# Kernel optimization log

Measured on AMD Instinct MI355X. Metric: run time of the kernel, lower is better.

The kernel has to match this reference:

```python
import jax, jax.numpy as jnp
import numpy as np

D_MODEL = 256
EXPERT_DIM = 512
NUM_EXPERTS = 8
TOP_K = 2
SEQ_LEN = 2048
BATCH = 2


def setup_inputs() -> dict:
    key = jax.random.key(0)
    ks = jax.random.split(key, 8)
    s = 0.02
    x = jax.random.normal(ks[0], (SEQ_LEN, BATCH, D_MODEL), dtype=jnp.float32)
    # gate: torch Linear(d_model, num_experts); store as [d, E] so logits = x @ Wg + bg
    Wg = jax.random.normal(ks[1], (D_MODEL, NUM_EXPERTS), dtype=jnp.float32) * s
    bg = jax.random.normal(ks[2], (NUM_EXPERTS,), dtype=jnp.float32) * s
    bias = jnp.zeros((NUM_EXPERTS,), dtype=jnp.float32)  # dynamic routing bias
    # experts: Linear(d, h) -> ReLU -> Linear(h, d), stacked over E
    W1 = jax.random.normal(ks[3], (NUM_EXPERTS, D_MODEL, EXPERT_DIM), dtype=jnp.float32) * s
    b1 = jax.random.normal(ks[4], (NUM_EXPERTS, EXPERT_DIM), dtype=jnp.float32) * s
    W2 = jax.random.normal(ks[5], (NUM_EXPERTS, EXPERT_DIM, D_MODEL), dtype=jnp.float32) * s
    b2 = jax.random.normal(ks[6], (NUM_EXPERTS, D_MODEL), dtype=jnp.float32) * s
    return {"x": x, "Wg": Wg, "bg": bg, "bias": bias, "W1": W1, "b1": b1, "W2": W2, "b2": b2}


def reference(x, Wg, bg, bias, W1, b1, W2, b2):
    # x: [seq, batch, d] -> flatten tokens
    x_flat = x.reshape(-1, D_MODEL)                      # [T, d]
    gate_logits = x_flat @ Wg + bg + bias                # [T, E]
    topk_vals, topk_idx = jax.lax.top_k(gate_logits, TOP_K)   # [T, K]
    # torch code subtracts the row max (topk_vals[:, :1], sorted desc) then softmaxes;
    # jax.nn.softmax is the same stable computation.
    topk_w = jax.nn.softmax(topk_vals, axis=-1)          # [T, K]
    # combine weights over experts: zero for unchosen experts -> exact same math
    # as the masked gather + scatter-add in the original loop.
    combine = (jax.nn.one_hot(topk_idx, NUM_EXPERTS, dtype=x.dtype)
               * topk_w[..., None]).sum(axis=1)          # [T, E]
    h = jax.nn.relu(jnp.einsum('td,edh->teh', x_flat, W1) + b1)   # [T, E, H]
    y = jnp.einsum('teh,ehd->ted', h, W2) + b2                     # [T, E, d]
    out = jnp.einsum('ted,te->td', y, combine)                     # [T, d]
    # dropout is identity in eval mode (p applied only in training)
    return out.reshape(x.shape)
```

## Files before the change

kernel.cpp:

```cpp
#include <hip/hip_runtime.h>
#include <hip/hip_bf16.h>
#include <math.h>

#define D_MODEL 256
#define EXPERT_DIM 512
#define NUM_EXPERTS 8
#define T_TOKENS 4096
#define TM 64
#define NGB 256
#define XS_LD 264

typedef unsigned short ushort_t;
typedef short short8_t __attribute__((ext_vector_type(8)));
typedef float f32x4 __attribute__((ext_vector_type(4)));

__device__ __forceinline__ ushort_t f2bf(float f) {
    unsigned int u = __float_as_uint(f);
    u += 0x7FFFu + ((u >> 16) & 1u);
    return (ushort_t)(u >> 16);
}
__device__ __forceinline__ float bf2f(ushort_t u) {
    return __uint_as_float((unsigned int)u << 16);
}

__global__ __launch_bounds__(256) void prep_kernel(
    const float* __restrict__ x, const float* __restrict__ Wg,
    const float* __restrict__ bg, const float* __restrict__ bias,
    const float* __restrict__ W1, const float* __restrict__ W2,
    ushort_t* __restrict__ W1f, ushort_t* __restrict__ W2f,
    ushort_t* __restrict__ xb,
    int* __restrict__ gcounts, int* __restrict__ lists,
    float* __restrict__ wts, int* __restrict__ slots)
{
    __shared__ int lcount[NUM_EXPERTS];
    const int tid = threadIdx.x;

    if (blockIdx.x < NGB) {
        const int gb = blockIdx.x;
        const int r = tid >> 4;
        const int c = tid & 15;
        const int t = gb * 16 + r;
        if (tid < NUM_EXPERTS) lcount[tid] = 0;

        float xr[16];
        const float4* xp = (const float4*)(x + (size_t)t * D_MODEL + c * 16);
#pragma unroll
        for (int q = 0; q < 4; ++q) {
            float4 v = xp[q];
            xr[q * 4 + 0] = v.x; xr[q * 4 + 1] = v.y;
            xr[q * 4 + 2] = v.z; xr[q * 4 + 3] = v.w;
        }
        ushort_t o16[16];
#pragma unroll
        for (int j = 0; j < 16; ++j) o16[j] = f2bf(xr[j]);
        ushort_t* xbp = xb + (size_t)t * D_MODEL + c * 16;
        *(int4*)(xbp)     = *(int4*)(o16);
        *(int4*)(xbp + 8) = *(int4*)(o16 + 8);

        float acc[NUM_EXPERTS];
#pragma unroll
        for (int e = 0; e < NUM_EXPERTS; ++e) acc[e] = 0.f;
#pragma unroll
        for (int j = 0; j < 16; ++j) {
            const float4* wg = (const float4*)(Wg + (c * 16 + j) * NUM_EXPERTS);
            float4 w0 = wg[0], w1 = wg[1];
            float xv = xr[j];
            acc[0] += xv * w0.x; acc[1] += xv * w0.y;
            acc[2] += xv * w0.z; acc[3] += xv * w0.w;
            acc[4] += xv * w1.x; acc[5] += xv * w1.y;
            acc[6] += xv * w1.z; acc[7] += xv * w1.w;
        }
#pragma unroll
        for (int e = 0; e < NUM_EXPERTS; ++e) {
#pragma unroll
            for (int s = 1; s < 16; s <<= 1) acc[e] += __shfl_xor(acc[e], s);
        }
        __syncthreads();
        if (c == 0) {
            float v0 = -3.0e38f, v1 = -3.0e38f; int i0 = 0, i1 = 0;
#pragma unroll
            for (int e = 0; e < NUM_EXPERTS; ++e) {
                float v = acc[e] + bg[e] + bias[e];
                if (v > v0) { v1 = v0; i1 = i0; v0 = v; i0 = e; }
                else if (v > v1) { v1 = v; i1 = e; }
            }
            float e1 = __expf(v1 - v0);
            float inv = 1.f / (1.f + e1);
            float w0 = inv, w1 = e1 * inv;

            int p0 = atomicAdd(&lcount[i0], 1);
            int p1 = atomicAdd(&lcount[i1], 1);
            lists[i0 * T_TOKENS + gb * 16 + p0] = t;
            wts  [i0 * T_TOKENS + gb * 16 + p0] = w0;
            lists[i1 * T_TOKENS + gb * 16 + p1] = t;
            wts  [i1 * T_TOKENS + gb * 16 + p1] = w1;
            slots[t] = (i0 << 12 | gb << 4 | p0) | ((i1 << 12 | gb << 4 | p1) << 16);
        }
        __syncthreads();
        if (tid < NUM_EXPERTS) gcounts[gb * NUM_EXPERTS + tid] = lcount[tid];
    } else {
        int gid = (blockIdx.x - NGB) * 256 + tid;
        bool isW2 = gid >= 131072;
        int idx = isW2 ? gid - 131072 : gid;
        int lane = idx & 63;
        int l15 = lane & 15, quad = lane >> 4;
        int ks = (idx >> 6) & 7;
        ushort_t o[8];
        if (!isW2) {
            int ntile = (idx >> 9) & 31, e = idx >> 14;
            int nn = ntile * 16 + l15;
            int k0 = ks * 32 + quad * 8;
            const float* s = W1 + ((size_t)e * D_MODEL + k0) * EXPERT_DIM + nn;
#pragma unroll
            for (int j = 0; j < 8; ++j) o[j] = f2bf(s[j * EXPERT_DIM]);
            *(int4*)(W1f + (size_t)idx * 8) = *(int4*)o;
        } else {
            int ntile = (idx >> 9) & 15, half = (idx >> 13) & 1, e = idx >> 14;
            int nn = ntile * 16 + l15;
            int k0 = half * 256 + ks * 32 + quad * 8;
            const float* s = W2 + ((size_t)e * EXPERT_DIM + k0) * D_MODEL + nn;
#pragma unroll
            for (int j = 0; j < 8; ++j) o[j] = f2bf(s[j * D_MODEL]);
            *(int4*)(W2f + (size_t)idx * 8) = *(int4*)o;
        }
    }
}

__global__ __launch_bounds__(256, 3) void moe_expert_mfma(
    const ushort_t* __restrict__ xb,
    const ushort_t* __restrict__ W1f, const float* __restrict__ b1,
    const ushort_t* __restrict__ W2f, const float* __restrict__ b2,
    const int* __restrict__ gcounts, const int* __restrict__ lists,
    const float* __restrict__ wts, ushort_t* __restrict__ ybuf)
{
    const int e = blockIdx.x;
    const int half = blockIdx.y;

    __shared__ ushort_t XH[TM * XS_LD];
    __shared__ int cum[257];
    __shared__ int wsums[4];
    __shared__ int   toks[TM];
    __shared__ float wt_s[TM];

    const int tid = threadIdx.x;
    const int lane = tid & 63;
    const int w = tid >> 6;
    const int l15 = lane & 15;
    const int quad = lane >> 4;

    {
        int v = gcounts[tid * NUM_EXPERTS + e];
#pragma unroll
        for (int s = 1; s < 64; s <<= 1) {
            int u = __shfl_up(v, s);
            if (lane >= s) v += u;
        }
        if (lane == 63) wsums[w] = v;
        __syncthreads();
        int off = 0;
        for (int i = 0; i < w; ++i) off += wsums[i];
        cum[tid + 1] = v + off;
        if (tid == 0) cum[0] = 0;
        __syncthreads();
    }
    const int n = cum[256];
    const int base = blockIdx.z * TM;
    if (base >= n) return;
    const int m = min(TM, n - base);

    if (tid < TM) {
        int p = base + tid;
        int tk = -1; float wv = 0.f;
        if (p < n) {
            int lo = 0;
#pragma unroll
            for (int s = 128; s >= 1; s >>= 1)
                if (cum[lo + s] <= p) lo += s;
            int idx = e * T_TOKENS + lo * 16 + (p - cum[lo]);
            tk = lists[idx]; wv = wts[idx];
        }
        toks[tid] = tk; wt_s[tid] = wv;
    }
    __syncthreads();

    for (int c = tid; c < TM * 32; c += 256) {
        int r = c >> 5, c8 = c & 31;
        int tk = toks[r];
        int4 v = make_int4(0, 0, 0, 0);
        if (tk >= 0) v = *(const int4*)(xb + (size_t)tk * D_MODEL + c8 * 8);
        *(int4*)(XH + r * XS_LD + c8 * 8) = v;
    }
    __syncthreads();

    const ushort_t* W1p = W1f + (size_t)(e * 32 + half * 16 + w * 4) * 4096 + lane * 8;
    float b1v[4];
#pragma unroll
    for (int nt = 0; nt < 4; ++nt)
        b1v[nt] = b1[e * EXPERT_DIM + half * 256 + w * 64 + nt * 16 + l15];

    f32x4 acc1[4][4] = {};
    short8_t bc[4];
#pragma unroll
    for (int nt = 0; nt < 4; ++nt) bc[nt] = *(const short8_t*)(W1p + nt * 4096);

    for (int ks = 0; ks < 8; ++ks) {
        short8_t bn[4];
        if (ks < 7) {
#pragma unroll
            for (int nt = 0; nt < 4; ++nt)
                bn[nt] = *(const short8_t*)(W1p + nt * 4096 + (ks + 1) * 512);
        }
        short8_t a[4];
#pragma unroll
        for (int mt = 0; mt < 4; ++mt)
            a[mt] = *(const short8_t*)(XH + (mt * 16 + l15) * XS_LD + ks * 32 + quad * 8);
#pragma unroll
        for (int mt = 0; mt < 4; ++mt)
#pragma unroll
            for (int nt = 0; nt < 4; ++nt)
                acc1[mt][nt] = __builtin_amdgcn_mfma_f32_16x16x32_bf16(
                    a[mt], bc[nt], acc1[mt][nt], 0, 0, 0);
        if (ks < 7) {
#pragma unroll
            for (int nt = 0; nt < 4; ++nt) bc[nt] = bn[nt];
        }
    }

    const ushort_t* W2p = W2f + (size_t)((e * 2 + half) * 16 + w * 4) * 4096 + lane * 8;
    short8_t bc2[4];
#pragma unroll
    for (int nt = 0; nt < 4; ++nt) bc2[nt] = *(const short8_t*)(W2p + nt * 4096);
    float b2v[4];
#pragma unroll
    for (int nt = 0; nt < 4; ++nt)
        b2v[nt] = half ? b2[e * D_MODEL + w * 64 + nt * 16 + l15] : 0.f;

    __syncthreads();
#pragma unroll
    for (int mt = 0; mt < 4; ++mt)
#pragma unroll
        for (int nt = 0; nt < 4; ++nt)
#pragma unroll
            for (int r = 0; r < 4; ++r) {
                int row = mt * 16 + quad * 4 + r;
                int col = w * 64 + nt * 16 + l15;
                float h = fmaxf(acc1[mt][nt][r] + b1v[nt], 0.f);
                XH[row * XS_LD + col] = f2bf(h);
            }
    __syncthreads();

    f32x4 acc2[4][4] = {};
    for (int ks = 0; ks < 8; ++ks) {
        short8_t bn2[4];
        if (ks < 7) {
#pragma unroll
            for (int nt = 0; nt < 4; ++nt)
                bn2[nt] = *(const short8_t*)(W2p + nt * 4096 + (ks + 1) * 512);
        }
        short8_t a[4];
#pragma unroll
        for (int mt = 0; mt < 4; ++mt)
            a[mt] = *(const short8_t*)(XH + (mt * 16 + l15) * XS_LD + ks * 32 + quad * 8);
#pragma unroll
        for (int mt = 0; mt < 4; ++mt)
#pragma unroll
            for (int nt = 0; nt < 4; ++nt)
                acc2[mt][nt] = __builtin_amdgcn_mfma_f32_16x16x32_bf16(
                    a[mt], bc2[nt], acc2[mt][nt], 0, 0, 0);
        if (ks < 7) {
#pragma unroll
            for (int nt = 0; nt < 4; ++nt) bc2[nt] = bn2[nt];
        }
    }

    ushort_t* yrow = ybuf + ((size_t)(half * NUM_EXPERTS + e) * T_TOKENS + base) * D_MODEL;
#pragma unroll
    for (int mt = 0; mt < 4; ++mt)
#pragma unroll
        for (int nt = 0; nt < 4; ++nt)
#pragma unroll
            for (int r = 0; r < 4; ++r) {
                int row = mt * 16 + quad * 4 + r;
                if (row < m) {
                    int col = w * 64 + nt * 16 + l15;
                    yrow[(size_t)row * D_MODEL + col] =
                        f2bf(wt_s[row] * (acc2[mt][nt][r] + b2v[nt]));
                }
            }
}

__global__ __launch_bounds__(256) void combine_kernel(
    const int* __restrict__ slots, const int* __restrict__ gcounts,
    const ushort_t* __restrict__ ybuf, float* __restrict__ out)
{
    __shared__ int cum8[NUM_EXPERTS][257];
    const int tid = threadIdx.x;
    const int lane = tid & 63;
    const int wv = tid >> 6;
#pragma unroll
    for (int rpt = 0; rpt < 2; ++rpt) {
        int e = wv + rpt * 4;
        int carry = 0;
        for (int ch = 0; ch < 4; ++ch) {
            int v = gcounts[(ch * 64 + lane) * NUM_EXPERTS + e];
#pragma unroll
            for (int s = 1; s < 64; s <<= 1) {
                int u = __shfl_up(v, s);
                if (lane >= s) v += u;
            }
            v += carry;
            cum8[e][ch * 64 + lane + 1] = v;
            carry = __shfl(v, 63);
        }
        if (lane == 0) cum8[e][0] = 0;
    }
    __syncthreads();

    int gid = blockIdx.x * 256 + tid;
    int t = gid >> 6;
    int sl = slots[t];
    int s0 = sl & 0xFFFF, s1 = (sl >> 16) & 0xFFFF;
    int e0 = (s0 >> 12) & 7, g0 = (s0 >> 4) & 255, lp0 = s0 & 15;
    int e1 = (s1 >> 12) & 7, g1 = (s1 >> 4) & 255, lp1 = s1 & 15;
    int p0 = cum8[e0][g0] + lp0;
    int p1 = cum8[e1][g1] + lp1;
    const size_t H = (size_t)NUM_EXPERTS * T_TOKENS * D_MODEL;
    size_t o0 = ((size_t)e0 * T_TOKENS + p0) * D_MODEL + lane * 4;
    size_t o1 = ((size_t)e1 * T_TOKENS + p1) * D_MODEL + lane * 4;
    ushort4 a = *(const ushort4*)(ybuf + o0);
    ushort4 b = *(const ushort4*)(ybuf + o0 + H);
    ushort4 c = *(const ushort4*)(ybuf + o1);
    ushort4 d = *(const ushort4*)(ybuf + o1 + H);
    float4 r;
    r.x = bf2f(a.x) + bf2f(b.x) + bf2f(c.x) + bf2f(d.x);
    r.y = bf2f(a.y) + bf2f(b.y) + bf2f(c.y) + bf2f(d.y);
    r.z = bf2f(a.z) + bf2f(b.z) + bf2f(c.z) + bf2f(d.z);
    r.w = bf2f(a.w) + bf2f(b.w) + bf2f(c.w) + bf2f(d.w);
    *(float4*)(out + (size_t)t * D_MODEL + lane * 4) = r;
}

extern "C" void kernel_launch(void* const* d_in, const int* in_sizes, int n_in,
                              void* d_out, int out_size, void* d_ws, size_t ws_size,
                              hipStream_t stream)
{
    const float* x    = (const float*)d_in[0];
    const float* Wg   = (const float*)d_in[1];
    const float* bg   = (const float*)d_in[2];
    const float* bias = (const float*)d_in[3];
    const float* W1   = (const float*)d_in[4];
    const float* b1   = (const float*)d_in[5];
    const float* W2   = (const float*)d_in[6];
    const float* b2   = (const float*)d_in[7];
    float* out = (float*)d_out;

    char* ws = (char*)d_ws;
    int*      gcounts = (int*)ws;
    int*      lists   = (int*)(ws + 8192);
    float*    wts     = (float*)(ws + 139264);
    int*      slots   = (int*)(ws + 270336);
    ushort_t* xb      = (ushort_t*)(ws + 524288);
    ushort_t* W1f     = (ushort_t*)(ws + 2621440);
    ushort_t* W2f     = (ushort_t*)(ws + 4718592);
    ushort_t* ybuf    = (ushort_t*)(ws + 6815744);

    prep_kernel<<<NGB + 1024, 256, 0, stream>>>(
        x, Wg, bg, bias, W1, W2, W1f, W2f, xb, gcounts, lists, wts, slots);

    moe_expert_mfma<<<dim3(NUM_EXPERTS, 2, T_TOKENS / TM), 256, 0, stream>>>(
        xb, W1f, b1, W2f, b2, gcounts, lists, wts, ybuf);

    combine_kernel<<<T_TOKENS * 64 / 256, 256, 0, stream>>>(slots, gcounts, ybuf, out);
}
```

Before: 104.6 us.

## Load gathered token rows directly into registers; batch tokens per combine block

The expert kernel no longer stages the gathered input tokens in shared memory. Each lane loads its A fragments straight from global memory through per-row pointers, with the next k-step prefetched, which removes a copy pass and a barrier. Invalid rows now read token 0 instead of zeros; their results appear to be discarded later. The combine kernel now has each block process 64 tokens (16 per wavefront), so it launches 64 blocks instead of 1024 and computes the per-expert prefix sums fewer times overall, at the cost of less parallelism.

```diff
diff --git a/kernel.cpp b/kernel.cpp
--- a/kernel.cpp
+++ b/kernel.cpp
@@ -136,7 +136,7 @@
     const int e = blockIdx.x;
     const int half = blockIdx.y;
 
-    __shared__ ushort_t XH[TM * XS_LD];
+    __shared__ ushort_t Hs[TM * XS_LD];
     __shared__ int cum[257];
     __shared__ int wsums[4];
     __shared__ int   toks[TM];
@@ -183,14 +183,12 @@
     }
     __syncthreads();
 
-    for (int c = tid; c < TM * 32; c += 256) {
-        int r = c >> 5, c8 = c & 31;
-        int tk = toks[r];
-        int4 v = make_int4(0, 0, 0, 0);
-        if (tk >= 0) v = *(const int4*)(xb + (size_t)tk * D_MODEL + c8 * 8);
-        *(int4*)(XH + r * XS_LD + c8 * 8) = v;
-    }
-    __syncthreads();
+    const ushort_t* arow[4];
+#pragma unroll
+    for (int mt = 0; mt < 4; ++mt) {
+        int tk = toks[mt * 16 + l15];
+        arow[mt] = xb + (size_t)(tk < 0 ? 0 : tk) * D_MODEL + quad * 8;
+    }
 
     const ushort_t* W1p = W1f + (size_t)(e * 32 + half * 16 + w * 4) * 4096 + lane * 8;
     float b1v[4];
@@ -199,30 +197,33 @@
         b1v[nt] = b1[e * EXPERT_DIM + half * 256 + w * 64 + nt * 16 + l15];
 
     f32x4 acc1[4][4] = {};
-    short8_t bc[4];
+    short8_t bc[4], ac[4];
 #pragma unroll
     for (int nt = 0; nt < 4; ++nt) bc[nt] = *(const short8_t*)(W1p + nt * 4096);
+#pragma unroll
+    for (int mt = 0; mt < 4; ++mt) ac[mt] = *(const short8_t*)(arow[mt]);
 
     for (int ks = 0; ks < 8; ++ks) {
-        short8_t bn[4];
+        short8_t bn[4], an[4];
         if (ks < 7) {
 #pragma unroll
             for (int nt = 0; nt < 4; ++nt)
                 bn[nt] = *(const short8_t*)(W1p + nt * 4096 + (ks + 1) * 512);
-        }
-        short8_t a[4];
-#pragma unroll
-        for (int mt = 0; mt < 4; ++mt)
-            a[mt] = *(const short8_t*)(XH + (mt * 16 + l15) * XS_LD + ks * 32 + quad * 8);
+#pragma unroll
+            for (int mt = 0; mt < 4; ++mt)
+                an[mt] = *(const short8_t*)(arow[mt] + (ks + 1) * 32);
+        }
 #pragma unroll
         for (int mt = 0; mt < 4; ++mt)
 #pragma unroll
             for (int nt = 0; nt < 4; ++nt)
                 acc1[mt][nt] = __builtin_amdgcn_mfma_f32_16x16x32_bf16(
-                    a[mt], bc[nt], acc1[mt][nt], 0, 0, 0);
+                    ac[mt], bc[nt], acc1[mt][nt], 0, 0, 0);
         if (ks < 7) {
 #pragma unroll
             for (int nt = 0; nt < 4; ++nt) bc[nt] = bn[nt];
+#pragma unroll
+            for (int mt = 0; mt < 4; ++mt) ac[mt] = an[mt];
         }
     }
 
@@ -235,7 +236,6 @@
     for (int nt = 0; nt < 4; ++nt)
         b2v[nt] = half ? b2[e * D_MODEL + w * 64 + nt * 16 + l15] : 0.f;
 
-    __syncthreads();
 #pragma unroll
     for (int mt = 0; mt < 4; ++mt)
 #pragma unroll
@@ -245,7 +245,7 @@
                 int row = mt * 16 + quad * 4 + r;
                 int col = w * 64 + nt * 16 + l15;
                 float h = fmaxf(acc1[mt][nt][r] + b1v[nt], 0.f);
-                XH[row * XS_LD + col] = f2bf(h);
+                Hs[row * XS_LD + col] = f2bf(h);
             }
     __syncthreads();
 
@@ -260,7 +260,7 @@
         short8_t a[4];
 #pragma unroll
         for (int mt = 0; mt < 4; ++mt)
-            a[mt] = *(const short8_t*)(XH + (mt * 16 + l15) * XS_LD + ks * 32 + quad * 8);
+            a[mt] = *(const short8_t*)(Hs + (mt * 16 + l15) * XS_LD + ks * 32 + quad * 8);
 #pragma unroll
         for (int mt = 0; mt < 4; ++mt)
 #pragma unroll
@@ -316,27 +316,29 @@
     }
     __syncthreads();
 
-    int gid = blockIdx.x * 256 + tid;
-    int t = gid >> 6;
-    int sl = slots[t];
-    int s0 = sl & 0xFFFF, s1 = (sl >> 16) & 0xFFFF;
-    int e0 = (s0 >> 12) & 7, g0 = (s0 >> 4) & 255, lp0 = s0 & 15;
-    int e1 = (s1 >> 12) & 7, g1 = (s1 >> 4) & 255, lp1 = s1 & 15;
-    int p0 = cum8[e0][g0] + lp0;
-    int p1 = cum8[e1][g1] + lp1;
     const size_t H = (size_t)NUM_EXPERTS * T_TOKENS * D_MODEL;
-    size_t o0 = ((size_t)e0 * T_TOKENS + p0) * D_MODEL + lane * 4;
-    size_t o1 = ((size_t)e1 * T_TOKENS + p1) * D_MODEL + lane * 4;
-    ushort4 a = *(const ushort4*)(ybuf + o0);
-    ushort4 b = *(const ushort4*)(ybuf + o0 + H);
-    ushort4 c = *(const ushort4*)(ybuf + o1);
-    ushort4 d = *(const ushort4*)(ybuf + o1 + H);
-    float4 r;
-    r.x = bf2f(a.x) + bf2f(b.x) + bf2f(c.x) + bf2f(d.x);
-    r.y = bf2f(a.y) + bf2f(b.y) + bf2f(c.y) + bf2f(d.y);
-    r.z = bf2f(a.z) + bf2f(b.z) + bf2f(c.z) + bf2f(d.z);
-    r.w = bf2f(a.w) + bf2f(b.w) + bf2f(c.w) + bf2f(d.w);
-    *(float4*)(out + (size_t)t * D_MODEL + lane * 4) = r;
+#pragma unroll
+    for (int it = 0; it < 16; ++it) {
+        int t = blockIdx.x * 64 + wv * 16 + it;
+        int sl = slots[t];
+        int s0 = sl & 0xFFFF, s1 = (sl >> 16) & 0xFFFF;
+        int e0 = (s0 >> 12) & 7, g0 = (s0 >> 4) & 255, lp0 = s0 & 15;
+        int e1 = (s1 >> 12) & 7, g1 = (s1 >> 4) & 255, lp1 = s1 & 15;
+        int p0 = cum8[e0][g0] + lp0;
+        int p1 = cum8[e1][g1] + lp1;
+        size_t o0 = ((size_t)e0 * T_TOKENS + p0) * D_MODEL + lane * 4;
+        size_t o1 = ((size_t)e1 * T_TOKENS + p1) * D_MODEL + lane * 4;
+        ushort4 a = *(const ushort4*)(ybuf + o0);
+        ushort4 b = *(const ushort4*)(ybuf + o0 + H);
+        ushort4 c = *(const ushort4*)(ybuf + o1);
+        ushort4 d = *(const ushort4*)(ybuf + o1 + H);
+        float4 r;
+        r.x = bf2f(a.x) + bf2f(b.x) + bf2f(c.x) + bf2f(d.x);
+        r.y = bf2f(a.y) + bf2f(b.y) + bf2f(c.y) + bf2f(d.y);
+        r.z = bf2f(a.z) + bf2f(b.z) + bf2f(c.z) + bf2f(d.z);
+        r.w = bf2f(a.w) + bf2f(b.w) + bf2f(c.w) + bf2f(d.w);
+        *(float4*)(out + (size_t)t * D_MODEL + lane * 4) = r;
+    }
 }
 
 extern "C" void kernel_launch(void* const* d_in, const int* in_sizes, int n_in,
@@ -369,5 +371,5 @@
     moe_expert_mfma<<<dim3(NUM_EXPERTS, 2, T_TOKENS / TM), 256, 0, stream>>>(
         xb, W1f, b1, W2f, b2, gcounts, lists, wts, ybuf);
 
-    combine_kernel<<<T_TOKENS * 64 / 256, 256, 0, stream>>>(slots, gcounts, ybuf, out);
-}
+    combine_kernel<<<T_TOKENS / 64, 256, 0, stream>>>(slots, gcounts, ybuf, out);
+}
```

Result: slower. 108.0 us (+3.3%).
